# Kernel optimization log

Measured on AMD Instinct MI355X. Metric: run time of the kernel, lower is better.

## Reference

```python
import jax, jax.numpy as jnp
import numpy as np
from math import sqrt

B, T, C, H = 4, 2048, 1024, 16
D = C // H  # head dim = 64


def setup_inputs() -> dict:
    key = jax.random.key(0)
    ks = jax.random.split(key, 9)
    s = 1.0 / sqrt(C)
    return {
        "x": jax.random.normal(ks[0], (B, T, C), dtype=jnp.float32),
        "Wk": jax.random.normal(ks[1], (C, C), dtype=jnp.float32) * s,
        "bk": jax.random.normal(ks[2], (C,), dtype=jnp.float32) * 0.01,
        "Wq": jax.random.normal(ks[3], (C, C), dtype=jnp.float32) * s,
        "bq": jax.random.normal(ks[4], (C,), dtype=jnp.float32) * 0.01,
        "Wv": jax.random.normal(ks[5], (C, C), dtype=jnp.float32) * s,
        "bv": jax.random.normal(ks[6], (C,), dtype=jnp.float32) * 0.01,
        "Wp": jax.random.normal(ks[7], (C, C), dtype=jnp.float32) * s,
        "bp": jax.random.normal(ks[8], (C,), dtype=jnp.float32) * 0.01,
    }


def reference(x, Wk, bk, Wq, bq, Wv, bv, Wp, bp):
    # Linear projections, split into heads: [B, H, T, D]
    def heads(y):
        return y.reshape(B, T, H, D).transpose(0, 2, 1, 3)

    k = heads(x @ Wk + bk)
    q = heads(x @ Wq + bq)
    v = heads(x @ Wv + bv)

    # scaled dot-product attention with causal mask (dropout p=0 -> identity)
    attn = jnp.einsum("bhtd,bhsd->bhts", q, k) / jnp.sqrt(jnp.float32(D))
    causal = jnp.tril(jnp.ones((T, T), dtype=bool))
    attn = jnp.where(causal[None, None], attn, -jnp.inf)
    attn = jax.nn.softmax(attn, axis=-1)

    y = jnp.einsum("bhts,bhsd->bhtd", attn, v)  # [B, H, T, D]
    y = y.transpose(0, 2, 1, 3).reshape(B, T, C)
    return y @ Wp + bp
```

## Files before the change

### kernel.cpp

```cpp
#include <hip/hip_runtime.h>
#include <hip/hip_bf16.h>
#include <math.h>


typedef short bf16x8 __attribute__((ext_vector_type(8)));
typedef float f32x4 __attribute__((ext_vector_type(4)));
typedef _Float16 f16x4 __attribute__((ext_vector_type(4)));

__device__ __forceinline__ short f2b(float f) {
    unsigned u = __float_as_uint(f);
    u = (u + 0x7fffu + ((u >> 16) & 1u)) >> 16;
    return (short)u;
}
__device__ __forceinline__ float b2f(short s) {
    return __uint_as_float(((unsigned)(unsigned short)s) << 16);
}

__global__ __launch_bounds__(256) void prep_kernel(const float* __restrict__ x, short* __restrict__ xb,
                                                   const float* W0, const float* W1,
                                                   const float* W2, const float* W3,
                                                   short* O0, short* O1, short* O2, short* O3) {
    int tid = threadIdx.x;
    if (blockIdx.x < 8192) {
        int idx = blockIdx.x * 256 + tid;
        float4 v = ((const float4*)x)[idx];
        short4 o;
        o.x = f2b(v.x); o.y = f2b(v.y); o.z = f2b(v.z); o.w = f2b(v.w);
        ((short4*)xb)[idx] = o;
        return;
    }
    int wid = blockIdx.x - 8192;
    const float* W; short* O;
    switch (wid >> 8) {
        case 0: W = W0; O = O0; break;
        case 1: W = W1; O = O1; break;
        case 2: W = W2; O = O2; break;
        default: W = W3; O = O3; break;
    }
    int rem = wid & 255;
    int n0 = (rem >> 4) * 64, k0 = (rem & 15) * 64;
    __shared__ __align__(16) float Ls[64 * 68];
    #pragma unroll
    for (int it = 0; it < 4; ++it) {
        int c = tid + it * 256;
        int r = c >> 4, off = (c & 15) * 4;
        *(float4*)&Ls[r * 68 + off] = *(const float4*)&W[(k0 + r) * 1024 + n0 + off];
    }
    __syncthreads();
    #pragma unroll
    for (int it = 0; it < 2; ++it) {
        int c = tid + it * 256;
        int n = c >> 3, koff = (c & 7) * 8;
        union { short s[8]; int4 v; } u;
        #pragma unroll
        for (int k = 0; k < 8; ++k) u.s[k] = f2b(Ls[(koff + k) * 68 + n]);
        *(int4*)&O[(n0 + n) * 1024 + k0 + koff] = u.v;
    }
}

template<int MODE>
__global__ __launch_bounds__(512, 2) void gemm8_kernel(const short* __restrict__ A,
                                                       const short* Bt0, const short* Bt1, const short* Bt2,
                                                       const float* b0, const float* b1, const float* b2,
                                                       float s0, float s1, float s2,
                                                       void* O0, void* O1, void* O2) {
    int z = blockIdx.z;
    const short* Bt   = (z == 0) ? Bt0 : (z == 1) ? Bt1 : Bt2;
    const float* bias = (z == 0) ? b0  : (z == 1) ? b1  : b2;
    float scl         = (z == 0) ? s0  : (z == 1) ? s1  : s2;
    void* Out         = (z == 0) ? O0  : (z == 1) ? O1  : O2;

    __shared__ __align__(16) short lds[73728];

    int tid = threadIdx.x;
    int w = tid >> 6, lane = tid & 63, quad = lane >> 4, l15 = lane & 15;
    int m0 = blockIdx.x * 128, n0 = blockIdx.y * 256;

    int srccol = ((lane & 3) * 8) ^ ((lane & 32) ? 16 : 0);
    const short* pA0 = A  + (m0 + w * 16 + (lane >> 2)) * 1024 + srccol;
    const short* pA1 = pA0 + 32;
    const short* pB0 = Bt + (n0 + (2 * w) * 16 + (lane >> 2)) * 1024 + srccol;
    const short* pB1 = pB0 + 32;
    const short* pB2 = pB0 + 16 * 1024;
    const short* pB3 = pB2 + 32;

    int dA = (w * 2) * 512;
    int dB = 24576 + (w * 4) * 512;

    int offR = l15 * 64 + ((quad * 16) ^ ((l15 & 8) << 2));
    int ma4 = (w >> 2) * 4;
    int nb2 = (w & 3) * 2;
    int jrow0 = nb2, jrow1 = nb2 + 1, jrow2 = nb2 + 8, jrow3 = nb2 + 9;
    const char* ldsb = (const char*)lds;

    f32x4 acc[4][4] = {};
    bf16x8 afA[4], bfA[4], afB[4], bfB[4];

#define STG(p, off) __builtin_amdgcn_global_load_lds( \
        (const __attribute__((address_space(1))) unsigned int*)(p), \
        (__attribute__((address_space(3))) unsigned int*)&lds[off], 16, 0, 0)
#define RD(base, row, kk) (*(const bf16x8*)(ldsb + (base) + ((row) * 2 + (kk)) * 1024 + offR))

    STG(pA0,      dA);                 STG(pA1,      dA + 512);
    STG(pB0,      dB);                 STG(pB1,      dB + 512);
    STG(pB2,      dB + 1024);          STG(pB3,      dB + 1536);
    STG(pA0 + 64, 8192 + dA);          STG(pA1 + 64, 8192 + dA + 512);
    STG(pB0 + 64, 16384 + dB);         STG(pB1 + 64, 16384 + dB + 512);
    STG(pB2 + 64, 16384 + dB + 1024);  STG(pB3 + 64, 16384 + dB + 1536);
    asm volatile("s_waitcnt vmcnt(6)" ::: "memory");
    __builtin_amdgcn_s_barrier();
    __builtin_amdgcn_sched_barrier(0);

    #pragma unroll
    for (int i = 0; i < 4; ++i) afA[i] = RD(0, ma4 + i, 0);
    bfA[0] = RD(49152, jrow0, 0); bfA[1] = RD(49152, jrow1, 0);
    bfA[2] = RD(49152, jrow2, 0); bfA[3] = RD(49152, jrow3, 0);

    #pragma unroll
    for (int t = 0; t < 16; ++t) {
        const int rs  = t % 3;
        const int rs1 = (t + 1) % 3;
        const int ss  = (t + 2) % 3;
        const int Ar  = rs * 16384;
        const int Br  = 49152 + rs * 32768;
        const int Ar1 = rs1 * 16384;
        const int Br1 = 49152 + rs1 * 32768;

        #pragma unroll
        for (int i = 0; i < 4; ++i) afB[i] = RD(Ar, ma4 + i, 1);
        bfB[0] = RD(Br, jrow0, 1); bfB[1] = RD(Br, jrow1, 1);
        bfB[2] = RD(Br, jrow2, 1); bfB[3] = RD(Br, jrow3, 1);
        if (t + 2 < 16) {
            STG(pA0 + (t + 2) * 64, ss * 8192 + dA);
            STG(pA1 + (t + 2) * 64, ss * 8192 + dA + 512);
            STG(pB0 + (t + 2) * 64, ss * 16384 + dB);
        }
        asm volatile("s_waitcnt lgkmcnt(8)" ::: "memory");
        __builtin_amdgcn_sched_barrier(0);
        __builtin_amdgcn_s_setprio(1);
        #pragma unroll
        for (int i = 0; i < 4; ++i)
            #pragma unroll
            for (int j = 0; j < 4; ++j)
                acc[i][j] = __builtin_amdgcn_mfma_f32_16x16x32_bf16(afA[i], bfA[j], acc[i][j], 0, 0, 0);
        __builtin_amdgcn_s_setprio(0);
        if (t < 14) {
            asm volatile("s_waitcnt vmcnt(3)" ::: "memory");
        } else if (t == 14) {
            asm volatile("s_waitcnt vmcnt(0)" ::: "memory");
        }
        __builtin_amdgcn_s_barrier();
        __builtin_amdgcn_sched_barrier(0);

        if (t < 15) {
            #pragma unroll
            for (int i = 0; i < 4; ++i) afA[i] = RD(Ar1, ma4 + i, 0);
            bfA[0] = RD(Br1, jrow0, 0); bfA[1] = RD(Br1, jrow1, 0);
            bfA[2] = RD(Br1, jrow2, 0); bfA[3] = RD(Br1, jrow3, 0);
        }
        if (t + 2 < 16) {
            STG(pB1 + (t + 2) * 64, ss * 16384 + dB + 512);
            STG(pB2 + (t + 2) * 64, ss * 16384 + dB + 1024);
            STG(pB3 + (t + 2) * 64, ss * 16384 + dB + 1536);
        }
        if (t < 15) {
            asm volatile("s_waitcnt lgkmcnt(8)" ::: "memory");
        } else {
            asm volatile("s_waitcnt lgkmcnt(0)" ::: "memory");
        }
        __builtin_amdgcn_sched_barrier(0);
        __builtin_amdgcn_s_setprio(1);
        #pragma unroll
        for (int i = 0; i < 4; ++i)
            #pragma unroll
            for (int j = 0; j < 4; ++j)
                acc[i][j] = __builtin_amdgcn_mfma_f32_16x16x32_bf16(afB[i], bfB[j], acc[i][j], 0, 0, 0);
        __builtin_amdgcn_s_setprio(0);
        if (t < 15) {
            __builtin_amdgcn_s_barrier();
            __builtin_amdgcn_sched_barrier(0);
        }
    }
#undef STG
#undef RD

    int mrow = m0 + (w >> 2) * 64;
    int ncol = n0 + (w & 3) * 32;
    #pragma unroll
    for (int i = 0; i < 4; ++i) {
        #pragma unroll
        for (int j = 0; j < 4; ++j) {
            int gn = ncol + (j >> 1) * 128 + (j & 1) * 16 + l15;
            float bv = bias[gn];
            if (MODE == 0 && z == 2) {
                int gm0 = mrow + i * 16 + quad * 4;
                int b = gm0 >> 11, tt = gm0 & 2047, h = gn >> 6, d = gn & 63;
                f16x4 hv;
                #pragma unroll
                for (int r = 0; r < 4; ++r) hv[r] = (_Float16)((acc[i][j][r] + bv) * scl);
                *(f16x4*)&((_Float16*)Out)[((b * 16 + h) * 64 + d) * 2048 + tt] = hv;
            } else {
                #pragma unroll
                for (int r = 0; r < 4; ++r) {
                    int gm = mrow + i * 16 + quad * 4 + r;
                    float v = (acc[i][j][r] + bv) * scl;
                    if (MODE == 0) {
                        int b = gm >> 11, tt = gm & 2047, h = gn >> 6, d = gn & 63;
                        ((short*)Out)[(((b * 16 + h) * 2048) + tt) * 64 + d] = f2b(v);
                    } else {
                        ((float*)Out)[gm * 1024 + gn] = v;
                    }
                }
            }
        }
    }
}

__global__ __launch_bounds__(256, 3) void attn_kernel(const short* __restrict__ Q,
                                                      const short* __restrict__ K,
                                                      const _Float16* __restrict__ Vt,
                                                      short* __restrict__ Y) {
    __shared__ __align__(16) short    Ks[128 * 64];
    __shared__ __align__(16) _Float16 Vs[64 * 128];

    int tid = threadIdx.x;
    int w = tid >> 6, lane = tid & 63, quad = lane >> 4, l15 = lane & 15;
    int idx = blockIdx.x;
    int qi = 15 - (idx >> 6);
    int bh = idx & 63;

    const short* Qh = Q + bh * 2048 * 64;
    const short* Kh = K + bh * 2048 * 64;
    const _Float16* Vh = Vt + bh * 64 * 2048;

    bf16x8 qf[2][2];
    #pragma unroll
    for (int i = 0; i < 2; ++i)
        #pragma unroll
        for (int kh = 0; kh < 2; ++kh) {
            int t = qi * 128 + w * 32 + i * 16 + l15;
            qf[i][kh] = *(const bf16x8*)&Qh[t * 64 + kh * 32 + quad * 8];
        }

    int krow = lane >> 3;
    int kchunk = ((lane & 7) ^ krow) * 8;
    int vrow = lane >> 4;
    int vchunk = ((lane & 15) ^ (w * 4 + vrow)) * 8;

    int t7 = l15 & 7;
    int kf0_off = ((quad ^ t7) * 8);
    int kf1_off = (((quad + 4) ^ t7) * 8);
    int vsub = (quad & 1) * 4;
    int vchi = quad >> 1;

    f32x4 o[2][4] = {};
    float lsum[2] = {0.f, 0.f};

    for (int si = 0; si <= qi; ++si) {
        const short* Kt = Kh + si * 128 * 64;
        const _Float16* Vtile = Vh + si * 128;
        bool diag = (si == qi);

        __syncthreads();
        #pragma unroll
        for (int it = 0; it < 4; ++it) {
            int kr0 = it * 32 + w * 8;
            __builtin_amdgcn_global_load_lds(
                (const __attribute__((address_space(1))) unsigned int*)&Kt[(kr0 + krow) * 64 + kchunk],
                (__attribute__((address_space(3))) unsigned int*)&Ks[kr0 * 64], 16, 0, 0);
            int vr0 = it * 16 + w * 4;
            __builtin_amdgcn_global_load_lds(
                (const __attribute__((address_space(1))) unsigned int*)&Vtile[(vr0 + vrow) * 2048 + vchunk],
                (__attribute__((address_space(3))) unsigned int*)&Vs[vr0 * 128], 16, 0, 0);
        }
        __syncthreads();

        #pragma unroll
        for (int j = 0; j < 8; ++j) {
            int trow = (j * 16 + l15) * 64;
            bf16x8 kf0 = *(const bf16x8*)&Ks[trow + kf0_off];
            bf16x8 kf1 = *(const bf16x8*)&Ks[trow + kf1_off];
            f16x4 pfv[2];
            #pragma unroll
            for (int i = 0; i < 2; ++i) {
                f32x4 a = {};
                a = __builtin_amdgcn_mfma_f32_16x16x32_bf16(kf0, qf[i][0], a, 0, 0, 0);
                a = __builtin_amdgcn_mfma_f32_16x16x32_bf16(kf1, qf[i][1], a, 0, 0, 0);
                if (diag) {
                    int qrel = w * 32 + i * 16 + l15;
                    #pragma unroll
                    for (int r = 0; r < 4; ++r)
                        if (j * 16 + quad * 4 + r > qrel) a[r] = -1e30f;
                }
                float p0 = __builtin_amdgcn_exp2f(a[0]);
                float p1 = __builtin_amdgcn_exp2f(a[1]);
                float p2 = __builtin_amdgcn_exp2f(a[2]);
                float p3 = __builtin_amdgcn_exp2f(a[3]);
                lsum[i] += (p0 + p1) + (p2 + p3);
                pfv[i][0] = (_Float16)p0;
                pfv[i][1] = (_Float16)p1;
                pfv[i][2] = (_Float16)p2;
                pfv[i][3] = (_Float16)p3;
            }
            int vc = (j * 2 + vchi);
            #pragma unroll
            for (int mt = 0; mt < 4; ++mt) {
                int d = mt * 16 + l15;
                f16x4 vf = *(const f16x4*)&Vs[d * 128 + ((vc ^ l15) * 8) + vsub];
                o[0][mt] = __builtin_amdgcn_mfma_f32_16x16x16f16(vf, pfv[0], o[0][mt], 0, 0, 0);
                o[1][mt] = __builtin_amdgcn_mfma_f32_16x16x16f16(vf, pfv[1], o[1][mt], 0, 0, 0);
            }
        }
    }

    int b = bh >> 4, h = bh & 15;
    #pragma unroll
    for (int i = 0; i < 2; ++i) {
        float l = lsum[i];
        l += __shfl_xor(l, 16);
        l += __shfl_xor(l, 32);
        float rinv = 1.0f / l;
        int q = qi * 128 + w * 32 + i * 16 + l15;
        short* yrow = &Y[(b * 2048 + q) * 1024 + h * 64];
        #pragma unroll
        for (int mt = 0; mt < 4; ++mt) {
            short4 s4;
            s4.x = f2b(o[i][mt][0] * rinv);
            s4.y = f2b(o[i][mt][1] * rinv);
            s4.z = f2b(o[i][mt][2] * rinv);
            s4.w = f2b(o[i][mt][3] * rinv);
            *(short4*)&yrow[mt * 16 + quad * 4] = s4;
        }
    }
}

extern "C" void kernel_launch(void* const* d_in, const int* in_sizes, int n_in,
                              void* d_out, int out_size, void* d_ws, size_t ws_size,
                              hipStream_t stream) {
    const float* x  = (const float*)d_in[0];
    const float* Wk = (const float*)d_in[1];
    const float* bk = (const float*)d_in[2];
    const float* Wq = (const float*)d_in[3];
    const float* bq = (const float*)d_in[4];
    const float* Wv = (const float*)d_in[5];
    const float* bv = (const float*)d_in[6];
    const float* Wp = (const float*)d_in[7];
    const float* bp = (const float*)d_in[8];

    char* ws = (char*)d_ws;
    short*     xb  = (short*)(ws + 0);
    short*     Wqt = (short*)(ws + 16777216);
    short*     Wkt = (short*)(ws + 18874368);
    short*     Wvt = (short*)(ws + 20971520);
    short*     Wpt = (short*)(ws + 23068672);
    short*     Qb  = (short*)(ws + 25165824);
    short*     Kb  = (short*)(ws + 41943040);
    _Float16*  Vtb = (_Float16*)(ws + 75497472);
    short*     Yb  = (short*)(ws + 92274688);

    prep_kernel<<<9216, 256, 0, stream>>>(x, xb, Wq, Wk, Wv, Wp, Wqt, Wkt, Wvt, Wpt);
    gemm8_kernel<0><<<dim3(64, 4, 3), 512, 0, stream>>>(xb, Wqt, Wkt, Wvt, bq, bk, bv,
                                                        0.18033688011112042f , 1.0f, 1.0f,
                                                        (void*)Qb, (void*)Kb, (void*)Vtb);
    attn_kernel<<<1024, 256, 0, stream>>>(Qb, Kb, Vtb, Yb);
    gemm8_kernel<1><<<dim3(64, 4, 1), 512, 0, stream>>>(Yb, Wpt, nullptr, nullptr,
                                                        bp, nullptr, nullptr,
                                                        1.0f, 1.0f, 1.0f,
                                                        (void*)d_out, nullptr, nullptr);
}
```

Before: 236.7 us.

## Double-buffer K/V tiles in attention kernel with async LDS prefetch

Doubles the shared-memory K and V tile buffers and issues the global-to-LDS loads for the next key tile before computing on the current one, using explicit vmcnt waits and barriers instead of __syncthreads around the loads. This is meant to hide global memory latency behind the MFMA work. In exchange, LDS use doubles, so the occupancy hint drops from 3 to 2 blocks per CU, which may reduce latency hiding across blocks.

```diff
diff --git a/kernel.cpp b/kernel.cpp
--- a/kernel.cpp
+++ b/kernel.cpp
@@ -216,12 +216,12 @@
     }
 }
 
-__global__ __launch_bounds__(256, 3) void attn_kernel(const short* __restrict__ Q,
+__global__ __launch_bounds__(256, 2) void attn_kernel(const short* __restrict__ Q,
                                                       const short* __restrict__ K,
                                                       const _Float16* __restrict__ Vt,
                                                       short* __restrict__ Y) {
-    __shared__ __align__(16) short    Ks[128 * 64];
-    __shared__ __align__(16) _Float16 Vs[64 * 128];
+    __shared__ __align__(16) short    Ks[2][128 * 64];
+    __shared__ __align__(16) _Float16 Vs[2][64 * 128];
 
     int tid = threadIdx.x;
     int w = tid >> 6, lane = tid & 63, quad = lane >> 4, l15 = lane & 15;
@@ -256,30 +256,46 @@
     f32x4 o[2][4] = {};
     float lsum[2] = {0.f, 0.f};
 
+    asm volatile("s_waitcnt vmcnt(0)" ::: "memory");
+    __builtin_amdgcn_sched_barrier(0);
+
+#define ASTAGE(si_, buf_) do { \
+    const short* Kt_ = Kh + (si_) * 128 * 64; \
+    const _Float16* Vt_ = Vh + (si_) * 128; \
+    _Pragma("unroll") \
+    for (int it = 0; it < 4; ++it) { \
+        int kr0 = it * 32 + w * 8; \
+        __builtin_amdgcn_global_load_lds( \
+            (const __attribute__((address_space(1))) unsigned int*)&Kt_[(kr0 + krow) * 64 + kchunk], \
+            (__attribute__((address_space(3))) unsigned int*)&Ks[buf_][kr0 * 64], 16, 0, 0); \
+        int vr0 = it * 16 + w * 4; \
+        __builtin_amdgcn_global_load_lds( \
+            (const __attribute__((address_space(1))) unsigned int*)&Vt_[(vr0 + vrow) * 2048 + vchunk], \
+            (__attribute__((address_space(3))) unsigned int*)&Vs[buf_][vr0 * 128], 16, 0, 0); \
+    } } while (0)
+
+    ASTAGE(0, 0);
+
     for (int si = 0; si <= qi; ++si) {
-        const short* Kt = Kh + si * 128 * 64;
-        const _Float16* Vtile = Vh + si * 128;
+        int buf = si & 1;
+        if (si < qi) {
+            ASTAGE(si + 1, buf ^ 1);
+            asm volatile("s_waitcnt vmcnt(8)" ::: "memory");
+        } else {
+            asm volatile("s_waitcnt vmcnt(0)" ::: "memory");
+        }
+        __builtin_amdgcn_s_barrier();
+        __builtin_amdgcn_sched_barrier(0);
+
+        const short* Ksb = Ks[buf];
+        const _Float16* Vsb = Vs[buf];
         bool diag = (si == qi);
-
-        __syncthreads();
-        #pragma unroll
-        for (int it = 0; it < 4; ++it) {
-            int kr0 = it * 32 + w * 8;
-            __builtin_amdgcn_global_load_lds(
-                (const __attribute__((address_space(1))) unsigned int*)&Kt[(kr0 + krow) * 64 + kchunk],
-                (__attribute__((address_space(3))) unsigned int*)&Ks[kr0 * 64], 16, 0, 0);
-            int vr0 = it * 16 + w * 4;
-            __builtin_amdgcn_global_load_lds(
-                (const __attribute__((address_space(1))) unsigned int*)&Vtile[(vr0 + vrow) * 2048 + vchunk],
-                (__attribute__((address_space(3))) unsigned int*)&Vs[vr0 * 128], 16, 0, 0);
-        }
-        __syncthreads();
 
         #pragma unroll
         for (int j = 0; j < 8; ++j) {
             int trow = (j * 16 + l15) * 64;
-            bf16x8 kf0 = *(const bf16x8*)&Ks[trow + kf0_off];
-            bf16x8 kf1 = *(const bf16x8*)&Ks[trow + kf1_off];
+            bf16x8 kf0 = *(const bf16x8*)&Ksb[trow + kf0_off];
+            bf16x8 kf1 = *(const bf16x8*)&Ksb[trow + kf1_off];
             f16x4 pfv[2];
             #pragma unroll
             for (int i = 0; i < 2; ++i) {
@@ -306,12 +322,17 @@
             #pragma unroll
             for (int mt = 0; mt < 4; ++mt) {
                 int d = mt * 16 + l15;
-                f16x4 vf = *(const f16x4*)&Vs[d * 128 + ((vc ^ l15) * 8) + vsub];
+                f16x4 vf = *(const f16x4*)&Vsb[d * 128 + ((vc ^ l15) * 8) + vsub];
                 o[0][mt] = __builtin_amdgcn_mfma_f32_16x16x16f16(vf, pfv[0], o[0][mt], 0, 0, 0);
                 o[1][mt] = __builtin_amdgcn_mfma_f32_16x16x16f16(vf, pfv[1], o[1][mt], 0, 0, 0);
             }
         }
-    }
+
+        asm volatile("s_waitcnt lgkmcnt(0)" ::: "memory");
+        __builtin_amdgcn_s_barrier();
+        __builtin_amdgcn_sched_barrier(0);
+    }
+#undef ASTAGE
 
     int b = bh >> 4, h = bh & 15;
     #pragma unroll
```

Result: no change. 237.1 us (+0.2%).
